# Kernel tuning notes

Measured on AMD Instinct MI355X. Metric: run time of the kernel, lower is better.

The kernel has to match this reference:

```python
import jax, jax.numpy as jnp
import numpy as np

N_NODES = 7
SIZE_X = 27
SIZE_X0 = 23
SIZE_H = 1024
SIZE_Z = 256
BATCH = 2048


def _gru(x, h, Wih, Whh, bih, bhh):
    # torch.nn.GRUCell math
    gi = x @ Wih.T + bih          # [B, 3H]
    gh = h @ Whh.T + bhh          # [B, 3H]
    ir, iz, inn = jnp.split(gi, 3, axis=-1)
    hr, hz, hn = jnp.split(gh, 3, axis=-1)
    r = jax.nn.sigmoid(ir + hr)
    z = jax.nn.sigmoid(iz + hz)
    n = jnp.tanh(inn + r * hn)
    return (1.0 - z) * n + z * h


def setup_inputs() -> dict:
    key = jax.random.key(0)
    ks = jax.random.split(key, 24)
    H, Xd, X0d, Zd = SIZE_H, SIZE_X, SIZE_X0, SIZE_Z

    def w(k, shape, fan):
        return jax.random.normal(k, shape, jnp.float32) / np.float32(np.sqrt(fan))

    inp = {}
    inp['X'] = jax.random.normal(ks[0], (BATCH, N_NODES, Xd), jnp.float32)
    inp['adj'] = jax.random.randint(ks[1], (BATCH, N_NODES, N_NODES), 0, 2, jnp.int32)
    # combin_encode GRUCell
    inp['W_ih_c'] = w(ks[2], (3 * H, Xd), H)
    inp['W_hh_c'] = w(ks[3], (3 * H, H), H)
    inp['b_ih_c'] = w(ks[4], (3 * H,), H)
    inp['b_hh_c'] = w(ks[5], (3 * H,), H)
    # loop_encode GRUCell
    inp['W_ih_l'] = w(ks[6], (3 * H, Xd), H)
    inp['W_hh_l'] = w(ks[7], (3 * H, H), H)
    inp['b_ih_l'] = w(ks[8], (3 * H,), H)
    inp['b_hh_l'] = w(ks[9], (3 * H,), H)
    # root_encode GRUCell (input size = size_X0)
    inp['W_ih_r'] = w(ks[10], (3 * H, X0d), H)
    inp['W_hh_r'] = w(ks[11], (3 * H, H), H)
    inp['b_ih_r'] = w(ks[12], (3 * H,), H)
    inp['b_hh_r'] = w(ks[13], (3 * H,), H)
    # gate: Linear(2H -> H) + sigmoid ; mapper: Linear(2H -> H, no bias)
    inp['Wg'] = w(ks[14], (H, 2 * H), 2 * H)
    inp['bg'] = w(ks[15], (H,), 2 * H)
    inp['Wm'] = w(ks[16], (H, 2 * H), 2 * H)
    # h_to_mu, h_to_std (Linear(H -> Z), std with softplus)
    inp['Wmu'] = w(ks[17], (Zd, H), H)
    inp['bmu'] = w(ks[18], (Zd,), H)
    inp['Wstd'] = w(ks[19], (Zd, H), H)
    inp['bstd'] = w(ks[20], (Zd,), H)
    return inp


def reference(X, adj,
              W_ih_c, W_hh_c, b_ih_c, b_hh_c,
              W_ih_l, W_hh_l, b_ih_l, b_hh_l,
              W_ih_r, W_hh_r, b_ih_r, b_hh_r,
              Wg, bg, Wm, Wmu, bmu, Wstd, bstd):
    B = X.shape[0]
    hidden = jnp.zeros((B, N_NODES, SIZE_H), X.dtype)
    # encode: nodes processed v = n-1 .. 0 (fixed small unrolled loop)
    for v in range(N_NODES - 1, -1, -1):
        if v == N_NODES - 1:
            H_in = jnp.zeros((B, SIZE_H), X.dtype)  # H_init = zeros
        else:
            H_nb = hidden[:, v + 1:, :]                    # [B, k, H] neighbors v+1..n-1
            pred = (adj[:, v + 1:, v] > 0)[..., None]       # edge x -> v
            succ = (adj[:, v, v + 1:] > 0)[..., None]       # edge v -> x
            Hcat = jnp.concatenate([jnp.where(pred, H_nb, 0.0),
                                    jnp.where(succ, H_nb, 0.0)], axis=-1)  # [B, k, 2H]
            g = jax.nn.sigmoid(jnp.einsum('bkf,hf->bkh', Hcat, Wg) + bg)
            m = jnp.einsum('bkf,hf->bkh', Hcat, Wm)
            H_in = (g * m).sum(axis=1)                      # gated sum over neighbors
        Xv = X[:, v]
        if v == 0:
            Hv = _gru(Xv[:, :SIZE_X0], H_in, W_ih_r, W_hh_r, b_ih_r, b_hh_r)
        else:
            Hv = _gru(Xv, H_in, W_ih_c, W_hh_c, b_ih_c, b_hh_c)
            self_loop = (adj[:, v, v] > 0)[:, None]
            X_loop = jnp.where(self_loop, Xv, 0.0)
            Hv = _gru(X_loop, Hv, W_ih_l, W_hh_l, b_ih_l, b_hh_l)
        hidden = hidden.at[:, v].set(Hv)
    Hg = hidden[:, 0]
    mu = Hg @ Wmu.T + bmu
    std = jax.nn.softplus(Hg @ Wstd.T + bstd)
    return mu, std
```

## Files before the change

kernel.cpp:

```cpp
#include <hip/hip_runtime.h>
#include <hip/hip_bf16.h>
#include <cmath>


typedef __hip_bfloat16 bf16;
typedef __attribute__((ext_vector_type(8))) short bf16x8;
typedef __attribute__((ext_vector_type(4))) float f32x4;

constexpr int BATCH = 2048;
constexpr int HD    = 1024;
constexpr int LDA   = 1056;
constexpr size_t BH = (size_t)BATCH * HD;

__device__ __forceinline__ bf16  f2bf(float v){ return __float2bfloat16(v); }
__device__ __forceinline__ float sigm(float x){ return 1.0f/(1.0f+__expf(-x)); }

__device__ __forceinline__ void async16(bf16* lds_base_wave_uniform, const bf16* g){
  __builtin_amdgcn_global_load_lds(
      (const __attribute__((address_space(1))) void*)g,
      (__attribute__((address_space(3))) void*)lds_base_wave_uniform, 16, 0, 0);
}
__device__ __forceinline__ void ld4f(const bf16* p, float* o){
  ushort4 u = *reinterpret_cast<const ushort4*>(p);
  o[0] = __uint_as_float(((unsigned)u.x)<<16);
  o[1] = __uint_as_float(((unsigned)u.y)<<16);
  o[2] = __uint_as_float(((unsigned)u.z)<<16);
  o[3] = __uint_as_float(((unsigned)u.w)<<16);
}
__device__ __forceinline__ void st4bf(bf16* p, const float* v){
  bf16 o[4] = {f2bf(v[0]), f2bf(v[1]), f2bf(v[2]), f2bf(v[3])};
  *reinterpret_cast<ushort4*>(p) = *reinterpret_cast<const ushort4*>(o);
}

__global__ __launch_bounds__(256) void pack_waug_i(
    const float* __restrict__ Whh, const float* __restrict__ Wih, int xw,
    bf16* __restrict__ out)
{
  int c = blockIdx.x;
  int h = c >> 2, g = c & 3;
  for (int ch = threadIdx.x; ch < 264; ch += 256){
    int f0 = ch*4;
    float v[4] = {0.f,0.f,0.f,0.f};
    if (f0 < 1024){
      if (g < 3){
        int src = (g==2) ? (2048+h) : (g*1024+h);
        const float4 t = *reinterpret_cast<const float4*>(Whh + (size_t)src*1024 + f0);
        v[0]=t.x; v[1]=t.y; v[2]=t.z; v[3]=t.w;
      }
    } else if (g != 2){
      int src = (g==0) ? h : (g==1) ? (1024+h) : (2048+h);
      int fx = f0 - 1024;
      #pragma unroll
      for (int j=0;j<4;++j) if (fx+j < xw) v[j] = Wih[(size_t)src*xw + fx + j];
    }
    st4bf(out + (size_t)c*LDA + f0, v);
  }
}

__global__ __launch_bounds__(256) void pack_wgm(const float* __restrict__ Wg,
    const float* __restrict__ Wm, bf16* __restrict__ outW){
  int i = blockIdx.x*256 + threadIdx.x;
  int c = i >> 8, f0 = (i & 255)*4;
  int j = c >> 10, h = c & 1023;
  const float* src = (j < 2) ? Wg : Wm;
  float4 t = *reinterpret_cast<const float4*>(src + (size_t)h*2048 + ((j & 1) ? 1024 : 0) + f0);
  float v[4] = {t.x,t.y,t.z,t.w};
  st4bf(outW + (size_t)c*1024 + f0, v);
}

__global__ __launch_bounds__(256) void pack_wms(const float* __restrict__ Wmu,
    const float* __restrict__ Wstd, bf16* __restrict__ outW){
  int i = blockIdx.x*256 + threadIdx.x;
  int c = i >> 8, f0 = (i & 255)*4;
  const float* src = (c < 256) ? (Wmu + (size_t)c*1024) : (Wstd + (size_t)(c-256)*1024);
  float4 t = *reinterpret_cast<const float4*>(src + f0);
  float v[4] = {t.x,t.y,t.z,t.w};
  st4bf(outW + (size_t)c*1024 + f0, v);
}

__global__ __launch_bounds__(256) void pack_xpad(const float* __restrict__ X,
    bf16* __restrict__ out){
  int i = blockIdx.x*256 + threadIdx.x;
  int f = i & 31, bv = i >> 5;
  int b = bv / 7, v = bv % 7;
  float val = (f < 27) ? X[((size_t)b*7 + v)*27 + f] : 0.f;
  out[((size_t)v*BATCH + b)*32 + f] = f2bf(val);
}
__global__ __launch_bounds__(256) void pack_xpr(const float* __restrict__ X,
    bf16* __restrict__ out){
  int i = blockIdx.x*256 + threadIdx.x;
  int f = i & 31, b = i >> 5;
  float val = (f < 23) ? X[(size_t)b*7*27 + f] : 0.f;
  out[(size_t)b*32 + f] = f2bf(val);
}

__global__ __launch_bounds__(256) void combine_k(
    const bf16* __restrict__ P, const int* __restrict__ adj,
    const float* __restrict__ bg, const bf16* __restrict__ tailsrc,
    bf16* __restrict__ Hin, int v)
{
  int t  = threadIdx.x;
  int b  = blockIdx.x*2 + (t>>7);
  int tl = t & 127;
  int h0 = tl*8;
  float acc[8] = {0,0,0,0,0,0,0,0};
  float bgv[8];
  { const float4 a = *reinterpret_cast<const float4*>(bg + h0);
    const float4 c = *reinterpret_cast<const float4*>(bg + h0 + 4);
    bgv[0]=a.x;bgv[1]=a.y;bgv[2]=a.z;bgv[3]=a.w;bgv[4]=c.x;bgv[5]=c.y;bgv[6]=c.z;bgv[7]=c.w; }
  for (int k=v+1;k<7;++k){
    bool p = adj[b*49 + k*7 + v] > 0;
    bool s = adj[b*49 + v*7 + k] > 0;
    if (!p && !s) continue;
    const bf16* base = P + (size_t)(k-1)*4*BH + (size_t)b*HD + h0;
    float g1[8], g2[8], m1[8], m2[8];
    ld4f(base,          g1); ld4f(base+4,        g1+4);
    ld4f(base+BH,       g2); ld4f(base+BH+4,     g2+4);
    ld4f(base+2*BH,     m1); ld4f(base+2*BH+4,   m1+4);
    ld4f(base+3*BH,     m2); ld4f(base+3*BH+4,   m2+4);
    #pragma unroll
    for (int u=0;u<8;++u){
      float gg = (p?g1[u]:0.f) + (s?g2[u]:0.f);
      float mm = (p?m1[u]:0.f) + (s?m2[u]:0.f);
      acc[u] += sigm(gg + bgv[u]) * mm;
    }
  }
  st4bf(Hin + (size_t)b*LDA + h0,     acc);
  st4bf(Hin + (size_t)b*LDA + h0 + 4, acc+4);
  if (tl < 4){
    const ushort4* s0 = reinterpret_cast<const ushort4*>(tailsrc + (size_t)b*32 + tl*8);
    ushort4* d0 = reinterpret_cast<ushort4*>(Hin + (size_t)b*LDA + 1024 + tl*8);
    d0[0] = s0[0]; d0[1] = s0[1];
  }
}

template<int MODE>
__global__ __launch_bounds__(256) void gemm_t(
    const bf16* __restrict__ A, const bf16* __restrict__ Bw,
    bf16* __restrict__ out, float* __restrict__ outF,
    const float* __restrict__ bias1, const float* __restrict__ bias2,
    const int* __restrict__ adj, const bf16* __restrict__ xpad,
    int lda, int ldb, int kb, int ktot, int v, int tailw)
{
  __shared__ __align__(16) bf16 S[64*136];
  bf16* As = S;
  bf16* Bs = S + 2048;
  const int tid  = threadIdx.x;
  const int rb0  = blockIdx.x*64, n0 = blockIdx.y*128;
  const int lane = tid & 63, w = tid >> 6;
  const int quad = lane >> 4, l15 = lane & 15;
  const int sr   = lane >> 2, sc = (lane & 3)*8;

  const bf16* gA = A  + (size_t)(rb0 + w*16 + sr)*lda + sc;
  const bf16* gB = Bw + (size_t)(n0  + w*32 + sr)*ldb + sc;
  bf16* lA = As + w*512;
  bf16* lB = Bs + w*1024;

  f32x4 acc[4][2] = {};
  for (int k0 = kb; k0 < ktot; k0 += 32){
    async16(lA,       gA + k0);
    async16(lB,       gB + k0);
    async16(lB + 512, gB + k0 + (size_t)16*ldb);
    __syncthreads();
    bf16x8 af0 = *reinterpret_cast<const bf16x8*>(&As[(  0 + l15)*32 + quad*8]);
    bf16x8 af1 = *reinterpret_cast<const bf16x8*>(&As[( 16 + l15)*32 + quad*8]);
    bf16x8 af2 = *reinterpret_cast<const bf16x8*>(&As[( 32 + l15)*32 + quad*8]);
    bf16x8 af3 = *reinterpret_cast<const bf16x8*>(&As[( 48 + l15)*32 + quad*8]);
    bf16x8 bf0 = *reinterpret_cast<const bf16x8*>(&Bs[w*1024 + (     l15)*32 + quad*8]);
    bf16x8 bf1 = *reinterpret_cast<const bf16x8*>(&Bs[w*1024 + (16 + l15)*32 + quad*8]);
    acc[0][0] = __builtin_amdgcn_mfma_f32_16x16x32_bf16(af0, bf0, acc[0][0], 0,0,0);
    acc[0][1] = __builtin_amdgcn_mfma_f32_16x16x32_bf16(af0, bf1, acc[0][1], 0,0,0);
    acc[1][0] = __builtin_amdgcn_mfma_f32_16x16x32_bf16(af1, bf0, acc[1][0], 0,0,0);
    acc[1][1] = __builtin_amdgcn_mfma_f32_16x16x32_bf16(af1, bf1, acc[1][1], 0,0,0);
    acc[2][0] = __builtin_amdgcn_mfma_f32_16x16x32_bf16(af2, bf0, acc[2][0], 0,0,0);
    acc[2][1] = __builtin_amdgcn_mfma_f32_16x16x32_bf16(af2, bf1, acc[2][1], 0,0,0);
    acc[3][0] = __builtin_amdgcn_mfma_f32_16x16x32_bf16(af3, bf0, acc[3][0], 0,0,0);
    acc[3][1] = __builtin_amdgcn_mfma_f32_16x16x32_bf16(af3, bf1, acc[3][1], 0,0,0);
    __syncthreads();
  }

  if (MODE == 1 || MODE == 2){
    #pragma unroll
    for (int tm=0;tm<4;++tm)
      #pragma unroll
      for (int tn=0;tn<2;++tn)
        #pragma unroll
        for (int i=0;i<4;++i){
          int b = rb0 + tm*16 + quad*4 + i;
          int c = n0  + w*32 + tn*16 + l15;
          float val = acc[tm][tn][i];
          if (MODE == 1){
            out[((size_t)(c>>10)*BATCH + b)*HD + (c & 1023)] = f2bf(val);
          } else {
            if (c < 256){
              outF[(size_t)b*256 + c] = val + bias1[c];
            } else {
              val += bias2[c-256];
              val = fmaxf(val,0.f) + log1pf(__expf(-fabsf(val)));
              outF[(size_t)BATCH*256 + (size_t)b*256 + (c-256)] = val;
            }
          }
        }
    return;
  }

  #pragma unroll
  for (int tm=0;tm<4;++tm)
    #pragma unroll
    for (int tn=0;tn<2;++tn)
      #pragma unroll
      for (int i=0;i<4;++i){
        int r = tm*16 + quad*4 + i;
        int c = w*32 + tn*16 + l15;
        S[r*136 + c] = f2bf(acc[tm][tn][i]);
      }
  __syncthreads();
  {
    const int row = tid >> 2;
    const int hs  = (tid & 3)*8;
    const int b   = rb0 + row;
    const int hbase = blockIdx.y*32;
    bf16 hv[16];
    #pragma unroll
    for (int j4=0; j4<8; j4+=4){
      const int hg = hbase + hs + j4;
      float4 bir = *reinterpret_cast<const float4*>(bias1 + hg);
      float4 biz = *reinterpret_cast<const float4*>(bias1 + 1024 + hg);
      float4 bin = *reinterpret_cast<const float4*>(bias1 + 2048 + hg);
      float4 bhr = *reinterpret_cast<const float4*>(bias2 + hg);
      float4 bhz = *reinterpret_cast<const float4*>(bias2 + 1024 + hg);
      float4 bhn = *reinterpret_cast<const float4*>(bias2 + 2048 + hg);
      const float* p_ir = &bir.x; const float* p_iz = &biz.x; const float* p_in = &bin.x;
      const float* p_hr = &bhr.x; const float* p_hz = &bhz.x; const float* p_hn = &bhn.x;
      float ho[4];
      ld4f(A + (size_t)b*lda + hg, ho);
      #pragma unroll
      for (int jj=0; jj<4; ++jj){
        float g[4];
        ld4f(&S[row*136 + (hs + j4 + jj)*4], g);
        float r = sigm(g[0] + p_ir[jj] + p_hr[jj]);
        float z = sigm(g[1] + p_iz[jj] + p_hz[jj]);
        float n = tanhf(g[3] + p_in[jj] + r*(g[2] + p_hn[jj]));
        hv[j4+jj] = f2bf((1.f - z)*n + z*ho[jj]);
      }
    }
    *reinterpret_cast<uint4*>(out + (size_t)b*lda + hbase + hs) =
        *reinterpret_cast<const uint4*>(&hv[0]);
  }
  if (tailw && blockIdx.y == 0){
    const int b = rb0 + (tid>>2), f0 = (tid&3)*8;
    bool self = adj[b*49 + v*8] > 0;
    uint4 tv = {0u,0u,0u,0u};
    if (self) tv = *reinterpret_cast<const uint4*>(xpad + (size_t)b*32 + f0);
    *reinterpret_cast<uint4*>(out + (size_t)b*lda + 1024 + f0) = tv;
  }
}

extern "C" void kernel_launch(void* const* d_in, const int* in_sizes, int n_in,
                              void* d_out, int out_size, void* d_ws, size_t ws_size,
                              hipStream_t stream)
{
  const float* X    = (const float*)d_in[0];
  const int*   adj  = (const int*)  d_in[1];
  const float* Wihc = (const float*)d_in[2];
  const float* Whhc = (const float*)d_in[3];
  const float* bihc = (const float*)d_in[4];
  const float* bhhc = (const float*)d_in[5];
  const float* Wihl = (const float*)d_in[6];
  const float* Whhl = (const float*)d_in[7];
  const float* bihl = (const float*)d_in[8];
  const float* bhhl = (const float*)d_in[9];
  const float* Wihr = (const float*)d_in[10];
  const float* Whhr = (const float*)d_in[11];
  const float* bihr = (const float*)d_in[12];
  const float* bhhr = (const float*)d_in[13];
  const float* Wg   = (const float*)d_in[14];
  const float* bg   = (const float*)d_in[15];
  const float* Wm   = (const float*)d_in[16];
  const float* Wmu  = (const float*)d_in[17];
  const float* bmu  = (const float*)d_in[18];
  const float* Wstd = (const float*)d_in[19];
  const float* bstd = (const float*)d_in[20];
  float* out = (float*)d_out;

  bf16* P    = (bf16*)d_ws;
  bf16* Hin  = P    + 24*BH;
  bf16* Hva  = Hin  + (size_t)BATCH*LDA;
  bf16* Hvb  = Hva  + (size_t)BATCH*LDA;
  bf16* Wca  = Hvb  + (size_t)BATCH*LDA;
  bf16* Wla  = Wca  + (size_t)4096*LDA;
  bf16* Wra  = Wla  + (size_t)4096*LDA;
  bf16* Wgm  = Wra  + (size_t)4096*LDA;
  bf16* Wms  = Wgm  + (size_t)4096*1024;
  bf16* Xp   = Wms  + (size_t)512*1024;
  bf16* XpR  = Xp   + (size_t)7*BATCH*32;

  pack_waug_i<<<4096, 256, 0, stream>>>(Whhc, Wihc, 27, Wca);
  pack_waug_i<<<4096, 256, 0, stream>>>(Whhl, Wihl, 27, Wla);
  pack_waug_i<<<4096, 256, 0, stream>>>(Whhr, Wihr, 23, Wra);
  pack_wgm  <<<4096, 256, 0, stream>>>(Wg, Wm, Wgm);
  pack_wms  <<<512,  256, 0, stream>>>(Wmu, Wstd, Wms);
  pack_xpad <<<1792, 256, 0, stream>>>(X, Xp);
  pack_xpr  <<<256,  256, 0, stream>>>(X, XpR);

  for (int v=6; v>=1; --v){
    const bf16* xt = Xp + (size_t)v*BATCH*32;
    combine_k<<<1024, 256, 0, stream>>>(P, adj, bg, xt, Hin, v);
    gemm_t<0><<<dim3(32,32), 256, 0, stream>>>(Hin, Wca, Hva, nullptr,
        bihc, bhhc, adj, xt, LDA, LDA, (v==6)?1024:0, 1056, v, 1);
    gemm_t<0><<<dim3(32,32), 256, 0, stream>>>(Hva, Wla, Hvb, nullptr,
        bihl, bhhl, adj, nullptr, LDA, LDA, 0, 1056, v, 0);
    gemm_t<1><<<dim3(32,32), 256, 0, stream>>>(Hvb, Wgm, P + (size_t)(v-1)*4*BH,
        nullptr, nullptr, nullptr, nullptr, nullptr, LDA, 1024, 0, 1024, 0, 0);
  }
  combine_k<<<1024, 256, 0, stream>>>(P, adj, bg, XpR, Hin, 0);
  gemm_t<0><<<dim3(32,32), 256, 0, stream>>>(Hin, Wra, Hva, nullptr,
      bihr, bhhr, adj, nullptr, LDA, LDA, 0, 1056, 0, 0);
  gemm_t<2><<<dim3(32,4), 256, 0, stream>>>(Hva, Wms, nullptr, out,
      bmu, bstd, nullptr, nullptr, LDA, 1024, 0, 1024, 0, 0);
}
```

Baseline: 840.7 us.

## Load MFMA fragments directly from global with register double-buffering and wider tiles

After: 1.095 ms. 30.3% more time.

```diff
diff --git a/kernel.cpp b/kernel.cpp
--- a/kernel.cpp
+++ b/kernel.cpp
@@ -15,11 +15,6 @@
 __device__ __forceinline__ bf16  f2bf(float v){ return __float2bfloat16(v); }
 __device__ __forceinline__ float sigm(float x){ return 1.0f/(1.0f+__expf(-x)); }
 
-__device__ __forceinline__ void async16(bf16* lds_base_wave_uniform, const bf16* g){
-  __builtin_amdgcn_global_load_lds(
-      (const __attribute__((address_space(1))) void*)g,
-      (__attribute__((address_space(3))) void*)lds_base_wave_uniform, 16, 0, 0);
-}
 __device__ __forceinline__ void ld4f(const bf16* p, float* o){
   ushort4 u = *reinterpret_cast<const ushort4*>(p);
   o[0] = __uint_as_float(((unsigned)u.x)<<16);
@@ -134,60 +129,68 @@
   }
 }
 
+#define LD8(dst, base, kk) dst = *reinterpret_cast<const bf16x8*>((base) + (kk))
+#define LOADALL(x0,x1,x2,x3,y0,y1,y2,y3,kk) do{ \
+  LD8(x0,pA0,kk); LD8(x1,pA1,kk); LD8(x2,pA2,kk); LD8(x3,pA3,kk); \
+  LD8(y0,pB0,kk); LD8(y1,pB1,kk); LD8(y2,pB2,kk); LD8(y3,pB3,kk); }while(0)
+#define MM(ar,bc,i,j) acc[i][j] = __builtin_amdgcn_mfma_f32_16x16x32_bf16(ar, bc, acc[i][j], 0,0,0)
+#define MFMA16(x0,x1,x2,x3,y0,y1,y2,y3) do{ \
+  MM(x0,y0,0,0); MM(x0,y1,0,1); MM(x0,y2,0,2); MM(x0,y3,0,3); \
+  MM(x1,y0,1,0); MM(x1,y1,1,1); MM(x1,y2,1,2); MM(x1,y3,1,3); \
+  MM(x2,y0,2,0); MM(x2,y1,2,1); MM(x2,y2,2,2); MM(x2,y3,2,3); \
+  MM(x3,y0,3,0); MM(x3,y1,3,1); MM(x3,y2,3,2); MM(x3,y3,3,3); }while(0)
+
 template<int MODE>
-__global__ __launch_bounds__(256) void gemm_t(
+__global__ __launch_bounds__(256) void gemm_dr(
     const bf16* __restrict__ A, const bf16* __restrict__ Bw,
     bf16* __restrict__ out, float* __restrict__ outF,
     const float* __restrict__ bias1, const float* __restrict__ bias2,
     const int* __restrict__ adj, const bf16* __restrict__ xpad,
     int lda, int ldb, int kb, int ktot, int v, int tailw)
 {
-  __shared__ __align__(16) bf16 S[64*136];
-  bf16* As = S;
-  bf16* Bs = S + 2048;
   const int tid  = threadIdx.x;
-  const int rb0  = blockIdx.x*64, n0 = blockIdx.y*128;
-  const int lane = tid & 63, w = tid >> 6;
+  const int rb0  = blockIdx.x*64;
+  const int w    = tid >> 6, lane = tid & 63;
   const int quad = lane >> 4, l15 = lane & 15;
-  const int sr   = lane >> 2, sc = (lane & 3)*8;
-
-  const bf16* gA = A  + (size_t)(rb0 + w*16 + sr)*lda + sc;
-  const bf16* gB = Bw + (size_t)(n0  + w*32 + sr)*ldb + sc;
-  bf16* lA = As + w*512;
-  bf16* lB = Bs + w*1024;
-
-  f32x4 acc[4][2] = {};
-  for (int k0 = kb; k0 < ktot; k0 += 32){
-    async16(lA,       gA + k0);
-    async16(lB,       gB + k0);
-    async16(lB + 512, gB + k0 + (size_t)16*ldb);
-    __syncthreads();
-    bf16x8 af0 = *reinterpret_cast<const bf16x8*>(&As[(  0 + l15)*32 + quad*8]);
-    bf16x8 af1 = *reinterpret_cast<const bf16x8*>(&As[( 16 + l15)*32 + quad*8]);
-    bf16x8 af2 = *reinterpret_cast<const bf16x8*>(&As[( 32 + l15)*32 + quad*8]);
-    bf16x8 af3 = *reinterpret_cast<const bf16x8*>(&As[( 48 + l15)*32 + quad*8]);
-    bf16x8 bf0 = *reinterpret_cast<const bf16x8*>(&Bs[w*1024 + (     l15)*32 + quad*8]);
-    bf16x8 bf1 = *reinterpret_cast<const bf16x8*>(&Bs[w*1024 + (16 + l15)*32 + quad*8]);
-    acc[0][0] = __builtin_amdgcn_mfma_f32_16x16x32_bf16(af0, bf0, acc[0][0], 0,0,0);
-    acc[0][1] = __builtin_amdgcn_mfma_f32_16x16x32_bf16(af0, bf1, acc[0][1], 0,0,0);
-    acc[1][0] = __builtin_amdgcn_mfma_f32_16x16x32_bf16(af1, bf0, acc[1][0], 0,0,0);
-    acc[1][1] = __builtin_amdgcn_mfma_f32_16x16x32_bf16(af1, bf1, acc[1][1], 0,0,0);
-    acc[2][0] = __builtin_amdgcn_mfma_f32_16x16x32_bf16(af2, bf0, acc[2][0], 0,0,0);
-    acc[2][1] = __builtin_amdgcn_mfma_f32_16x16x32_bf16(af2, bf1, acc[2][1], 0,0,0);
-    acc[3][0] = __builtin_amdgcn_mfma_f32_16x16x32_bf16(af3, bf0, acc[3][0], 0,0,0);
-    acc[3][1] = __builtin_amdgcn_mfma_f32_16x16x32_bf16(af3, bf1, acc[3][1], 0,0,0);
-    __syncthreads();
+  const int n0w  = blockIdx.y*256 + w*64;
+
+  const bf16* pA0 = A + (size_t)(rb0 + l15)*lda + quad*8;
+  const bf16* pA1 = pA0 + (size_t)16*lda;
+  const bf16* pA2 = pA0 + (size_t)32*lda;
+  const bf16* pA3 = pA0 + (size_t)48*lda;
+  const bf16* pB0 = Bw + (size_t)(n0w + l15)*ldb + quad*8;
+  const bf16* pB1 = pB0 + (size_t)16*ldb;
+  const bf16* pB2 = pB0 + (size_t)32*ldb;
+  const bf16* pB3 = pB0 + (size_t)48*ldb;
+
+  f32x4 acc[4][4] = {};
+  bf16x8 a0,a1,a2,a3,b0,b1,b2,b3;
+  bf16x8 p0,p1,p2,p3,q0,q1,q2,q3;
+
+  int k = kb;
+  const int nk = (ktot - kb) >> 5;
+  LOADALL(a0,a1,a2,a3,b0,b1,b2,b3, k);
+  if (nk & 1){
+    MFMA16(a0,a1,a2,a3,b0,b1,b2,b3);
+    k += 32;
+    if (k < ktot) LOADALL(a0,a1,a2,a3,b0,b1,b2,b3, k);
+  }
+  for (; k + 32 < ktot; k += 64){
+    LOADALL(p0,p1,p2,p3,q0,q1,q2,q3, k+32);
+    MFMA16(a0,a1,a2,a3,b0,b1,b2,b3);
+    if (k + 64 < ktot) LOADALL(a0,a1,a2,a3,b0,b1,b2,b3, k+64);
+    MFMA16(p0,p1,p2,p3,q0,q1,q2,q3);
   }
 
   if (MODE == 1 || MODE == 2){
     #pragma unroll
     for (int tm=0;tm<4;++tm)
       #pragma unroll
-      for (int tn=0;tn<2;++tn)
+      for (int tn=0;tn<4;++tn)
         #pragma unroll
         for (int i=0;i<4;++i){
           int b = rb0 + tm*16 + quad*4 + i;
-          int c = n0  + w*32 + tn*16 + l15;
+          int c = n0w + tn*16 + l15;
           float val = acc[tm][tn][i];
           if (MODE == 1){
             out[((size_t)(c>>10)*BATCH + b)*HD + (c & 1023)] = f2bf(val);
@@ -204,26 +207,27 @@
     return;
   }
 
+  __shared__ __align__(16) bf16 S[64*264];
   #pragma unroll
   for (int tm=0;tm<4;++tm)
     #pragma unroll
-    for (int tn=0;tn<2;++tn)
+    for (int tn=0;tn<4;++tn)
       #pragma unroll
       for (int i=0;i<4;++i){
         int r = tm*16 + quad*4 + i;
-        int c = w*32 + tn*16 + l15;
-        S[r*136 + c] = f2bf(acc[tm][tn][i]);
+        int c = w*64 + tn*16 + l15;
+        S[r*264 + c] = f2bf(acc[tm][tn][i]);
       }
   __syncthreads();
   {
     const int row = tid >> 2;
-    const int hs  = (tid & 3)*8;
+    const int hs  = (tid & 3)*16;
     const int b   = rb0 + row;
-    const int hbase = blockIdx.y*32;
+    const int hb  = blockIdx.y*64;
     bf16 hv[16];
     #pragma unroll
-    for (int j4=0; j4<8; j4+=4){
-      const int hg = hbase + hs + j4;
+    for (int j4=0; j4<16; j4+=4){
+      const int hg = hb + hs + j4;
       float4 bir = *reinterpret_cast<const float4*>(bias1 + hg);
       float4 biz = *reinterpret_cast<const float4*>(bias1 + 1024 + hg);
       float4 bin = *reinterpret_cast<const float4*>(bias1 + 2048 + hg);
@@ -237,15 +241,16 @@
       #pragma unroll
       for (int jj=0; jj<4; ++jj){
         float g[4];
-        ld4f(&S[row*136 + (hs + j4 + jj)*4], g);
+        ld4f(&S[row*264 + (hs + j4 + jj)*4], g);
         float r = sigm(g[0] + p_ir[jj] + p_hr[jj]);
         float z = sigm(g[1] + p_iz[jj] + p_hz[jj]);
         float n = tanhf(g[3] + p_in[jj] + r*(g[2] + p_hn[jj]));
         hv[j4+jj] = f2bf((1.f - z)*n + z*ho[jj]);
       }
     }
-    *reinterpret_cast<uint4*>(out + (size_t)b*lda + hbase + hs) =
-        *reinterpret_cast<const uint4*>(&hv[0]);
+    uint4* dst = reinterpret_cast<uint4*>(out + (size_t)b*lda + hb + hs);
+    dst[0] = *reinterpret_cast<const uint4*>(&hv[0]);
+    dst[1] = *reinterpret_cast<const uint4*>(&hv[8]);
   }
   if (tailw && blockIdx.y == 0){
     const int b = rb0 + (tid>>2), f0 = (tid&3)*8;
@@ -306,16 +311,16 @@
   for (int v=6; v>=1; --v){
     const bf16* xt = Xp + (size_t)v*BATCH*32;
     combine_k<<<1024, 256, 0, stream>>>(P, adj, bg, xt, Hin, v);
-    gemm_t<0><<<dim3(32,32), 256, 0, stream>>>(Hin, Wca, Hva, nullptr,
+    gemm_dr<0><<<dim3(32,16), 256, 0, stream>>>(Hin, Wca, Hva, nullptr,
         bihc, bhhc, adj, xt, LDA, LDA, (v==6)?1024:0, 1056, v, 1);
-    gemm_t<0><<<dim3(32,32), 256, 0, stream>>>(Hva, Wla, Hvb, nullptr,
+    gemm_dr<0><<<dim3(32,16), 256, 0, stream>>>(Hva, Wla, Hvb, nullptr,
         bihl, bhhl, adj, nullptr, LDA, LDA, 0, 1056, v, 0);
-    gemm_t<1><<<dim3(32,32), 256, 0, stream>>>(Hvb, Wgm, P + (size_t)(v-1)*4*BH,
+    gemm_dr<1><<<dim3(32,16), 256, 0, stream>>>(Hvb, Wgm, P + (size_t)(v-1)*4*BH,
         nullptr, nullptr, nullptr, nullptr, nullptr, LDA, 1024, 0, 1024, 0, 0);
   }
   combine_k<<<1024, 256, 0, stream>>>(P, adj, bg, XpR, Hin, 0);
-  gemm_t<0><<<dim3(32,32), 256, 0, stream>>>(Hin, Wra, Hva, nullptr,
+  gemm_dr<0><<<dim3(32,16), 256, 0, stream>>>(Hin, Wra, Hva, nullptr,
       bihr, bhhr, adj, nullptr, LDA, LDA, 0, 1056, 0, 0);
-  gemm_t<2><<<dim3(32,4), 256, 0, stream>>>(Hva, Wms, nullptr, out,
+  gemm_dr<2><<<dim3(32,2), 256, 0, stream>>>(Hva, Wms, nullptr, out,
       bmu, bstd, nullptr, nullptr, LDA, 1024, 0, 1024, 0, 0);
 }
```
